# Performance work log

Hardware: AMD Instinct MI355X
Metric: run time of the kernel (lower is better)

The kernel has to match this reference:

```python
import jax, jax.numpy as jnp
import numpy as np

PATCH_LENGTH = 200

def setup_inputs() -> dict:
    key = jax.random.key(0)
    eeg_input = jax.random.normal(key, (16, 32, 1000, 64), dtype=jnp.float32)
    return {"eeg_input": eeg_input}

def reference(eeg_input):
    # eeg_input: [B, W, T, C]
    B, W, T, C = eeg_input.shape
    nt = T // PATCH_LENGTH  # number of time patches per channel
    T_used = nt * PATCH_LENGTH
    # Torch loops iterate ch_idx (outer), t_idx (inner) -> channel-major patch order.
    # [B, W, T, C] -> [B, W, C, T] -> [B, W, C, nt, P] -> [B, W, C*nt, P]
    x = jnp.transpose(eeg_input[:, :, :T_used, :], (0, 1, 3, 2))
    patches = x.reshape(B, W, C * nt, PATCH_LENGTH)
    channel_indices = jnp.repeat(jnp.arange(C, dtype=jnp.int64), nt)  # [C*nt]
    time_indices = jnp.tile(jnp.arange(nt, dtype=jnp.int64), C)       # [C*nt]
    return patches, channel_indices, time_indices
```

## Files before the change

### kernel.cpp

```cpp
#include <hip/hip_runtime.h>


#define TDIM 1000
#define CDIM 64
#define TT   100
#define LSTR 65
#define NTILE 10
#define PATCH_ELEMS 32768000

typedef float v4f __attribute__((ext_vector_type(4)));

__global__ __launch_bounds__(320) void labram_patcher_kernel(
    const float* __restrict__ in, float* __restrict__ out)
{
    __shared__ float lds[TT * LSTR];

    const int tid  = threadIdx.x;
    const int tile = blockIdx.x % NTILE;
    const int bw   = blockIdx.x / NTILE;
    const int t0   = tile * TT;

    const v4f* in4 = (const v4f*)(in + (size_t)(bw * TDIM + t0) * CDIM);
    v4f v[5];
#pragma unroll
    for (int k = 0; k < 5; ++k)
        v[k] = in4[tid + 320 * k];
#pragma unroll
    for (int k = 0; k < 5; ++k) {
        int idx = tid + 320 * k;
        int ti  = idx >> 4;
        int c4  = idx & 15;
        int base = ti * LSTR + c4 * 4;
        lds[base + 0] = v[k].x;
        lds[base + 1] = v[k].y;
        lds[base + 2] = v[k].z;
        lds[base + 3] = v[k].w;
    }
    __syncthreads();

    v4f o[5];
    int cc[5], jj[5];
#pragma unroll
    for (int k = 0; k < 5; ++k) {
        int idx = tid + 320 * k;
        int c   = idx / 25;
        int j   = idx - c * 25;
        int ti  = j * 4;
        cc[k] = c; jj[k] = j;
        o[k].x = lds[(ti + 0) * LSTR + c];
        o[k].y = lds[(ti + 1) * LSTR + c];
        o[k].z = lds[(ti + 2) * LSTR + c];
        o[k].w = lds[(ti + 3) * LSTR + c];
    }
#pragma unroll
    for (int k = 0; k < 5; ++k) {
        size_t off = (size_t)(bw * CDIM + cc[k]) * TDIM + (t0 + jj[k] * 4);
        __builtin_nontemporal_store(o[k], (v4f*)(out + off));
    }

    if (blockIdx.x == 0) {
        out[PATCH_ELEMS + tid]       = (float)(tid / 5);
        out[PATCH_ELEMS + 320 + tid] = (float)(tid % 5);
    }
}

extern "C" void kernel_launch(void* const* d_in, const int* in_sizes, int n_in,
                              void* d_out, int out_size, void* d_ws, size_t ws_size,
                              hipStream_t stream) {
    const float* in = (const float*)d_in[0];
    float* out = (float*)d_out;
    dim3 grid(512 * NTILE);
    dim3 block(320);
    labram_patcher_kernel<<<grid, block, 0, stream>>>(in, out);
}
```

Before: 251.4 us.

## Split tile into per-wave LDS slices and replace block barrier with wave barrier

```diff
diff --git a/kernel.cpp b/kernel.cpp
--- a/kernel.cpp
+++ b/kernel.cpp
@@ -3,8 +3,9 @@
 
 #define TDIM 1000
 #define CDIM 64
-#define TT   100
 #define LSTR 65
+#define WROWS 20
+#define WSLICE (WROWS * LSTR)
 #define NTILE 10
 #define PATCH_ELEMS 32768000
 
@@ -13,49 +14,51 @@
 __global__ __launch_bounds__(320) void labram_patcher_kernel(
     const float* __restrict__ in, float* __restrict__ out)
 {
-    __shared__ float lds[TT * LSTR];
+    __shared__ float lds[5 * WSLICE];
 
     const int tid  = threadIdx.x;
+    const int lane = tid & 63;
+    const int w    = tid >> 6;
     const int tile = blockIdx.x % NTILE;
     const int bw   = blockIdx.x / NTILE;
-    const int t0   = tile * TT;
+    const int t0   = tile * 100 + w * WROWS;
 
-    const v4f* in4 = (const v4f*)(in + (size_t)(bw * TDIM + t0) * CDIM);
+    float* slice = lds + w * WSLICE;
+
+    const v4f* in4 = (const v4f*)in + (size_t)(bw * TDIM + t0) * (CDIM / 4);
     v4f v[5];
 #pragma unroll
     for (int k = 0; k < 5; ++k)
-        v[k] = in4[tid + 320 * k];
+        v[k] = in4[lane + 64 * k];
 #pragma unroll
     for (int k = 0; k < 5; ++k) {
-        int idx = tid + 320 * k;
+        int idx = lane + 64 * k;
         int ti  = idx >> 4;
         int c4  = idx & 15;
-        int base = ti * LSTR + c4 * 4;
-        lds[base + 0] = v[k].x;
-        lds[base + 1] = v[k].y;
-        lds[base + 2] = v[k].z;
-        lds[base + 3] = v[k].w;
+        float* p = slice + ti * LSTR + c4 * 4;
+        p[0] = v[k].x; p[1] = v[k].y; p[2] = v[k].z; p[3] = v[k].w;
     }
-    __syncthreads();
+
+    __builtin_amdgcn_wave_barrier();
 
     v4f o[5];
     int cc[5], jj[5];
 #pragma unroll
     for (int k = 0; k < 5; ++k) {
-        int idx = tid + 320 * k;
-        int c   = idx / 25;
-        int j   = idx - c * 25;
-        int ti  = j * 4;
+        int idx = lane + 64 * k;
+        int c   = idx / 5;
+        int j   = idx - 5 * c;
         cc[k] = c; jj[k] = j;
-        o[k].x = lds[(ti + 0) * LSTR + c];
-        o[k].y = lds[(ti + 1) * LSTR + c];
-        o[k].z = lds[(ti + 2) * LSTR + c];
-        o[k].w = lds[(ti + 3) * LSTR + c];
+        int b = (j * 4) * LSTR + c;
+        o[k].x = slice[b];
+        o[k].y = slice[b + LSTR];
+        o[k].z = slice[b + 2 * LSTR];
+        o[k].w = slice[b + 3 * LSTR];
     }
 #pragma unroll
     for (int k = 0; k < 5; ++k) {
         size_t off = (size_t)(bw * CDIM + cc[k]) * TDIM + (t0 + jj[k] * 4);
-        __builtin_nontemporal_store(o[k], (v4f*)(out + off));
+        *(v4f*)(out + off) = o[k];
     }
 
     if (blockIdx.x == 0) {
```

Result: slower. 260.2 us (+3.5%).
